# Optimization experiments

Measured on AMD Instinct MI355X. Metric: run time of the kernel, lower is better.

## Reference

```python
import jax, jax.numpy as jnp
import numpy as np

B, S, D, H = 2, 2048, 1024, 16
d = D // H          # per-head dim (chunk along feature dim)
SEQ_LEN = 1024      # config.seq_len mask width
SCALE = float(np.sqrt(D))  # post-softmax divide by sqrt(model_dimension)
LN_EPS = 1e-5


def setup_inputs() -> dict:
    key = jax.random.key(0)
    ks = jax.random.split(key, 10)
    init = lambda k, shape: (jax.random.normal(k, shape, dtype=jnp.float32) * 0.02)
    return {
        "x": jax.random.normal(ks[0], (B, S, D), dtype=jnp.float32),
        "Wq": init(ks[1], (H, d, d)), "bq": jnp.zeros((H, d), jnp.float32),
        "Wk": init(ks[2], (H, d, d)), "bk": jnp.zeros((H, d), jnp.float32),
        "Wv": init(ks[3], (H, d, d)), "bv": jnp.zeros((H, d), jnp.float32),
        "Wo": init(ks[4], (D, D)),    "bo": jnp.zeros((D,), jnp.float32),
        "ln_g": jnp.ones((D,), jnp.float32),
        "ln_b": jnp.zeros((D,), jnp.float32),
    }


def reference(x, Wq, bq, Wk, bk, Wv, bv, Wo, bo, ln_g, ln_b):
    # chunk along feature dim == reshape D -> (H, d) since chunks are contiguous
    xh = x.reshape(B, S, H, d)                                  # [B,S,H,d]
    q = jnp.einsum('bshd,hde->bshe', xh, Wq) + bq               # [B,S,H,d]
    k = jnp.einsum('bshd,hde->bshe', xh, Wk) + bk
    v = jnp.einsum('bshd,hde->bshe', xh, Wv) + bv
    scores = jnp.einsum('bshd,bthd->bhst', q, k)                # [B,H,S,S]
    # custom mask: last query row, last SEQ_LEN key columns -> -inf
    scores = scores.at[:, :, -1, -SEQ_LEN:].set(-jnp.inf)
    attn = jax.nn.softmax(scores, axis=-1) / SCALE              # post-softmax scale
    o = jnp.einsum('bhst,bthd->bshd', attn, v).reshape(B, S, D) # concat heads
    proj = jnp.einsum('bsd,de->bse', o, Wo) + bo                # output projection
    y = x + proj                                                 # residual
    mu = jnp.mean(y, axis=-1, keepdims=True)
    var = jnp.mean(jnp.square(y - mu), axis=-1, keepdims=True)
    return (y - mu) * jax.lax.rsqrt(var + LN_EPS) * ln_g + ln_b
```

## Files before the change

kernel.cpp:

```cpp
#include <hip/hip_runtime.h>
#include <math.h>

#define B 2
#define S 2048
#define D 1024
#define H 16
#define HD 64
#define LN_EPS 1e-5f
#define LOG2E 1.44269504f
#define KSPLIT 2
#define NTS (S / 64 / KSPLIT)
#define NBD_ELEMS (B * S * D)
#define BHS_ELEMS (B * H * S)

typedef __bf16 bf16x8 __attribute__((ext_vector_type(8)));
typedef float f32x4 __attribute__((ext_vector_type(4)));

#if defined(__has_builtin)
#if __has_builtin(__builtin_amdgcn_exp2f)
#define EXP2(x) __builtin_amdgcn_exp2f(x)
#endif
#endif
#ifndef EXP2
#define EXP2(x) __expf((x) * 0.6931471805599453f)
#endif

__device__ __forceinline__ ushort f2bf(float f) {
    uint u = __float_as_uint(f);
    u += 0x7FFFu + ((u >> 16) & 1u);
    return (ushort)(u >> 16);
}

__device__ __forceinline__ bf16x8 ldfrag(const char* base, int row, int cbyte) {
    int a = row * 128 + (cbyte ^ ((row & 7) << 4));
    union { uint4 u; bf16x8 v; } c;
    c.u = *(const uint4*)(base + a);
    return c.v;
}

__device__ __forceinline__ uint comb2(uint a, uint b, float inv) {
    float lo = (__uint_as_float(a << 16) + __uint_as_float(b << 16)) * inv;
    float hi = (__uint_as_float(a & 0xFFFF0000u) + __uint_as_float(b & 0xFFFF0000u)) * inv;
    return (uint)f2bf(lo) | ((uint)f2bf(hi) << 16);
}

__global__ __launch_bounds__(256) void cvt_kernel(
        const float* __restrict__ Wo,
        const float* __restrict__ Wq, const float* __restrict__ Wk,
        const float* __restrict__ Wv,
        ushort* __restrict__ wt, ushort* __restrict__ wqt,
        ushort* __restrict__ wkt, ushort* __restrict__ wvt) {
    __shared__ float t[64][65];
    int tid = threadIdx.x;
    if (blockIdx.y < 16) {
        int r0 = blockIdx.y * 64, c0 = blockIdx.x * 64;
#pragma unroll
        for (int it = 0; it < 16; ++it) {
            int idx = tid + 256 * it;
            int row = idx >> 6, col = idx & 63;
            t[row][col] = Wo[(size_t)(r0 + row) * D + c0 + col];
        }
        __syncthreads();
#pragma unroll
        for (int it = 0; it < 16; ++it) {
            int idx = tid + 256 * it;
            int nrow = idx >> 6, kcol = idx & 63;
            wt[(size_t)(c0 + nrow) * D + r0 + kcol] = f2bf(t[kcol][nrow]);
        }
    } else {
        int h = blockIdx.x, which = blockIdx.y - 16;
        const float* W = (which == 0) ? Wq : (which == 1) ? Wk : Wv;
        ushort* outp = (which == 0) ? wqt : (which == 1) ? wkt : wvt;
        const float* Wh = W + h * HD * HD;
        ushort* oh = outp + h * HD * HD;
#pragma unroll
        for (int it = 0; it < 16; ++it) {
            int idx = tid + 256 * it;
            t[idx >> 6][idx & 63] = Wh[idx];
        }
        __syncthreads();
#pragma unroll
        for (int it = 0; it < 16; ++it) {
            int idx = tid + 256 * it;
            int e = idx >> 6, dd = idx & 63;
            oh[idx] = f2bf(t[dd][e]);
        }
    }
}

__global__ __launch_bounds__(256) void qkv_kernel(
        const float* __restrict__ x,
        const ushort* __restrict__ wqt, const ushort* __restrict__ wkt,
        const ushort* __restrict__ wvt,
        const float* __restrict__ bq, const float* __restrict__ bk,
        const float* __restrict__ bv,
        ushort* __restrict__ qh, ushort* __restrict__ kh, ushort* __restrict__ vth) {
    __shared__ char xt[16384];
    const int tid = threadIdx.x;
    const int w = tid >> 6, l = tid & 63;
    const int lg = l >> 4, lr = l & 15;
    const int h = blockIdx.y;
    const size_t row0 = (size_t)blockIdx.x * 128;
    const int b = (int)(row0 >> 11);
    const int s0 = (int)(row0 & (S - 1));
    const size_t hb = (size_t)b * H + h;

#pragma unroll
    for (int it = 0; it < 4; ++it) {
        int c = tid + 256 * it;
        int row = c >> 3, sub = c & 7;
        const float* src = x + (row0 + row) * D + h * HD + 8 * sub;
        float4 f0 = *(const float4*)src;
        float4 f1 = *(const float4*)(src + 4);
        uint2 lo = make_uint2((uint)f2bf(f0.x) | ((uint)f2bf(f0.y) << 16),
                              (uint)f2bf(f0.z) | ((uint)f2bf(f0.w) << 16));
        uint2 hi = make_uint2((uint)f2bf(f1.x) | ((uint)f2bf(f1.y) << 16),
                              (uint)f2bf(f1.z) | ((uint)f2bf(f1.w) << 16));
        int p0 = 64 * (sub >> 2) + 32 * (sub & 1) + 8 * ((sub >> 1) & 1);
        int sz = (row & 7) << 4;
        char* dst = xt + row * 128;
        *(uint2*)(dst + (p0 ^ sz)) = lo;
        *(uint2*)(dst + ((p0 + 16) ^ sz)) = hi;
    }
    __syncthreads();

    bf16x8 xa[2][2];
#pragma unroll
    for (int fm = 0; fm < 2; ++fm)
#pragma unroll
        for (int ks = 0; ks < 2; ++ks)
            xa[fm][ks] = ldfrag(xt, 32 * w + 16 * fm + lr, 64 * ks + 16 * lg);

#pragma unroll
    for (int tsel = 0; tsel < 3; ++tsel) {
        const ushort* wsrc = (tsel == 0) ? wqt : (tsel == 1) ? wkt : wvt;
        const float* bsrc = (tsel == 0) ? bq : (tsel == 1) ? bk : bv;
        bf16x8 wf[4][2];
#pragma unroll
        for (int fn = 0; fn < 4; ++fn) {
            const char* wp = (const char*)(wsrc + ((size_t)h * HD + 16 * fn + lr) * HD);
#pragma unroll
            for (int ks = 0; ks < 2; ++ks) {
                uint2 a = *(const uint2*)(wp + 64 * ks + 8 * lg);
                uint2 c2 = *(const uint2*)(wp + 64 * ks + 8 * lg + 32);
                union { uint4 u; bf16x8 v; } cc;
                cc.u = make_uint4(a.x, a.y, c2.x, c2.y);
                wf[fn][ks] = cc.v;
            }
        }
        f32x4 acc[2][4];
#pragma unroll
        for (int fm = 0; fm < 2; ++fm)
#pragma unroll
            for (int fn = 0; fn < 4; ++fn)
#pragma unroll
                for (int r = 0; r < 4; ++r) acc[fm][fn][r] = 0.f;
#pragma unroll
        for (int fm = 0; fm < 2; ++fm)
#pragma unroll
            for (int fn = 0; fn < 4; ++fn)
#pragma unroll
                for (int ks = 0; ks < 2; ++ks)
                    acc[fm][fn] = __builtin_amdgcn_mfma_f32_16x16x32_bf16(
                        xa[fm][ks], wf[fn][ks], acc[fm][fn], 0, 0, 0);
        if (tsel == 0) {
#pragma unroll
            for (int fn = 0; fn < 4; ++fn) {
                float bias = bsrc[h * HD + 16 * fn + lr];
#pragma unroll
                for (int fm = 0; fm < 2; ++fm)
#pragma unroll
                    for (int r = 0; r < 4; ++r) {
                        int srow = s0 + 32 * w + 16 * fm + 4 * lg + r;
                        qh[(hb * S + srow) * HD + 16 * fn + lr] =
                            f2bf((acc[fm][fn][r] + bias) * LOG2E);
                    }
            }
        } else if (tsel == 1) {
#pragma unroll
            for (int fn = 0; fn < 4; ++fn) {
                float bias = bsrc[h * HD + 16 * fn + lr];
#pragma unroll
                for (int fm = 0; fm < 2; ++fm)
#pragma unroll
                    for (int r = 0; r < 4; ++r) {
                        int srow = s0 + 32 * w + 16 * fm + 4 * lg + r;
                        kh[(hb * S + srow) * HD + 16 * fn + lr] =
                            f2bf(acc[fm][fn][r] + bias);
                    }
            }
        } else {
#pragma unroll
            for (int fn = 0; fn < 4; ++fn) {
                float bias = bsrc[h * HD + 16 * fn + lr];
                int e = 16 * fn + lr;
#pragma unroll
                for (int fm = 0; fm < 2; ++fm) {
                    uint2 pk;
                    pk.x = (uint)f2bf(acc[fm][fn][0] + bias) |
                           ((uint)f2bf(acc[fm][fn][1] + bias) << 16);
                    pk.y = (uint)f2bf(acc[fm][fn][2] + bias) |
                           ((uint)f2bf(acc[fm][fn][3] + bias) << 16);
                    *(uint2*)(vth + (hb * HD + e) * S + s0 + 32 * w + 16 * fm + 4 * lg) = pk;
                }
            }
        }
    }
}

__global__ __launch_bounds__(256) void attn_kernel(
        const ushort* __restrict__ qh, const ushort* __restrict__ kh,
        const ushort* __restrict__ vth, ushort* __restrict__ ou,
        float* __restrict__ ls) {
    __shared__ char kt[3][8192];
    __shared__ char vt[3][8192];
    const int tid = threadIdx.x;
    const int w = tid >> 6, l = tid & 63;
    const int lg = l >> 4, lr = l & 15;
    const int flat = blockIdx.x + 8 * (blockIdx.y + 2 * blockIdx.z);
    const int xc = flat & 7, sl = flat >> 3;
    const int g = xc + 8 * (sl & 7);
    const int qi = sl >> 3;
    const int ksp = g >> 5;
    const int h = g & (H - 1), b = (g >> 4) & 1;
    const int q0 = qi * 256 + 64 * w;
    const size_t bh = (size_t)b * H + h;
    const ushort* qbase = qh + bh * S * HD;
    const ushort* kbase = kh + bh * S * HD;
    const ushort* vbase = vth + bh * HD * S;

    const int r0s = tid >> 3, ssub = tid & 7;
    const int sp0 = 64 * (ssub >> 2) + 32 * (ssub & 1) + 8 * ((ssub >> 1) & 1);
    const int ssz = (r0s & 7) << 4;

    bf16x8 qf[4][2];
#pragma unroll
    for (int fn = 0; fn < 4; ++fn) {
        const char* qp = (const char*)(qbase + (size_t)(q0 + 16 * fn + lr) * HD);
#pragma unroll
        for (int ks = 0; ks < 2; ++ks) {
            uint2 xlo = *(const uint2*)(qp + 64 * ks + 8 * lg);
            uint2 xhi = *(const uint2*)(qp + 64 * ks + 8 * lg + 32);
            union { uint4 u; bf16x8 v; } c;
            c.u = make_uint4(xlo.x, xlo.y, xhi.x, xhi.y);
            qf[fn][ks] = c.v;
        }
    }

    f32x4 acc[4][4];
#pragma unroll
    for (int fn = 0; fn < 4; ++fn)
#pragma unroll
        for (int n0 = 0; n0 < 4; ++n0)
#pragma unroll
            for (int r = 0; r < 4; ++r) acc[fn][n0][r] = 0.f;
    f32x4 accs[4];
#pragma unroll
    for (int fn = 0; fn < 4; ++fn)
#pragma unroll
        for (int r = 0; r < 4; ++r) accs[fn][r] = 0.f;
    const f32x4 z4 = {0.f, 0.f, 0.f, 0.f};
    bf16x8 onef;
#pragma unroll
    for (int j = 0; j < 8; ++j) onef[j] = (__bf16)1.0f;
    const bool lastq = (q0 + 64 == S) && (lr == 15);

    {
        const int kv0 = ksp * NTS * 64;
#pragma unroll
        for (int it = 0; it < 2; ++it) {
            int row = r0s + 32 * it;
            uint4 kd = *(const uint4*)(kbase + (size_t)(kv0 + row) * HD + 8 * ssub);
            uint4 vd = *(const uint4*)(vbase + (size_t)row * S + kv0 + 8 * ssub);
            char* kr = kt[0] + row * 128;
            char* vr = vt[0] + row * 128;
            *(uint2*)(kr + (sp0 ^ ssz)) = make_uint2(kd.x, kd.y);
            *(uint2*)(kr + ((sp0 + 16) ^ ssz)) = make_uint2(kd.z, kd.w);
            *(uint2*)(vr + (sp0 ^ ssz)) = make_uint2(vd.x, vd.y);
            *(uint2*)(vr + ((sp0 + 16) ^ ssz)) = make_uint2(vd.z, vd.w);
        }
    }
    __syncthreads();

    int cur = 0;
    for (int t = 0; t < NTS; ++t) {
        const int kv0 = (ksp * NTS + t) * 64;
        int nxt = cur + 1; if (nxt == 3) nxt = 0;
        uint4 kd2[2], vd2[2];
        if (t + 1 < NTS) {
#pragma unroll
            for (int it = 0; it < 2; ++it) {
                int row = r0s + 32 * it;
                kd2[it] = *(const uint4*)(kbase + (size_t)(kv0 + 64 + row) * HD + 8 * ssub);
                vd2[it] = *(const uint4*)(vbase + (size_t)row * S + kv0 + 64 + 8 * ssub);
            }
        }

        const char* ktb = kt[cur];
        const char* vtb = vt[cur];
        __builtin_amdgcn_s_setprio(1);
        bf16x8 pa[4][2];
#pragma unroll
        for (int half = 0; half < 2; ++half) {
            f32x4 s2[2][4];
#pragma unroll
            for (int fm2 = 0; fm2 < 2; ++fm2) {
                int fm = 2 * half + fm2;
                bf16x8 k0 = ldfrag(ktb, fm * 16 + lr, 16 * lg);
                bf16x8 k1 = ldfrag(ktb, fm * 16 + lr, 64 + 16 * lg);
#pragma unroll
                for (int fn = 0; fn < 4; ++fn) {
                    s2[fm2][fn] = __builtin_amdgcn_mfma_f32_16x16x32_bf16(k0, qf[fn][0], z4, 0, 0, 0);
                    s2[fm2][fn] = __builtin_amdgcn_mfma_f32_16x16x32_bf16(k1, qf[fn][1], s2[fm2][fn], 0, 0, 0);
                }
            }
            if (lastq && kv0 >= S - 1024) {
#pragma unroll
                for (int fm2 = 0; fm2 < 2; ++fm2)
#pragma unroll
                    for (int r = 0; r < 4; ++r) s2[fm2][3][r] = -INFINITY;
            }
#pragma unroll
            for (int fn = 0; fn < 4; ++fn)
#pragma unroll
                for (int j = 0; j < 8; ++j)
                    pa[fn][half][j] = (__bf16)EXP2(s2[j >> 2][fn][j & 3]);
        }
#pragma unroll
        for (int fn = 0; fn < 4; ++fn) {
            accs[fn] = __builtin_amdgcn_mfma_f32_16x16x32_bf16(pa[fn][0], onef, accs[fn], 0, 0, 0);
            accs[fn] = __builtin_amdgcn_mfma_f32_16x16x32_bf16(pa[fn][1], onef, accs[fn], 0, 0, 0);
        }
#pragma unroll
        for (int n0 = 0; n0 < 4; ++n0) {
            bf16x8 v0 = ldfrag(vtb, n0 * 16 + lr, 16 * lg);
            bf16x8 v1 = ldfrag(vtb, n0 * 16 + lr, 64 + 16 * lg);
#pragma unroll
            for (int fn = 0; fn < 4; ++fn) {
                acc[fn][n0] = __builtin_amdgcn_mfma_f32_16x16x32_bf16(pa[fn][0], v0, acc[fn][n0], 0, 0, 0);
                acc[fn][n0] = __builtin_amdgcn_mfma_f32_16x16x32_bf16(pa[fn][1], v1, acc[fn][n0], 0, 0, 0);
            }
        }
        __builtin_amdgcn_s_setprio(0);

        if (t + 1 < NTS) {
#pragma unroll
            for (int it = 0; it < 2; ++it) {
                int row = r0s + 32 * it;
                char* kr = kt[nxt] + row * 128;
                char* vr = vt[nxt] + row * 128;
                *(uint2*)(kr + (sp0 ^ ssz)) = make_uint2(kd2[it].x, kd2[it].y);
                *(uint2*)(kr + ((sp0 + 16) ^ ssz)) = make_uint2(kd2[it].z, kd2[it].w);
                *(uint2*)(vr + (sp0 ^ ssz)) = make_uint2(vd2[it].x, vd2[it].y);
                *(uint2*)(vr + ((sp0 + 16) ^ ssz)) = make_uint2(vd2[it].z, vd2[it].w);
            }
            __syncthreads();
        }
        cur = nxt;
    }

#pragma unroll
    for (int fn = 0; fn < 4; ++fn)
#pragma unroll
        for (int r = 0; r < 4; ++r) {
            int qrow = q0 + 16 * fn + 4 * lg + r;
            ushort* op = ou + (((size_t)ksp * B + b) * S + qrow) * D + h * HD;
#pragma unroll
            for (int n0 = 0; n0 < 4; ++n0)
                op[n0 * 16 + lr] = f2bf(acc[fn][n0][r]);
            if (lr == 0)
                ls[(((size_t)ksp * B + b) * H + h) * S + qrow] = accs[fn][r];
        }
}

__global__ __launch_bounds__(256) void proj_gemm_kernel(
        const ushort* __restrict__ ou, const float* __restrict__ ls,
        const ushort* __restrict__ wt,
        const float* __restrict__ x, const float* __restrict__ bo,
        float* __restrict__ yws) {
    __shared__ char at[3][8192];
    __shared__ char btl[3][16384];
    const int tid = threadIdx.x;
    const int w = tid >> 6, l = tid & 63;
    const int lg = l >> 4, lr = l & 15;
    const int wr = w >> 1, wc = w & 1;
    const int flat = blockIdx.x + 8 * blockIdx.y;
    const int xc = flat & 7, sl = flat >> 3;
    const int m0 = (xc + 8 * (sl & 7)) * 64;
    const int n0 = (sl >> 3) * 128;

    const ushort* srcA[2];
    const float* lsp[2];
    int offA1[2], offA2[2];
#pragma unroll
    for (int it = 0; it < 2; ++it) {
        int c = tid + 256 * it;
        int row = c >> 3, sub = c & 7;
        int r = m0 + row;
        srcA[it] = ou + (size_t)r * D + 8 * sub;
        int b = r >> 11, s = r & (S - 1);
        lsp[it] = ls + (size_t)b * H * S + s;
        int p0 = 64 * (sub >> 2) + 32 * (sub & 1) + 8 * ((sub >> 1) & 1);
        int sz = (row & 7) << 4;
        offA1[it] = row * 128 + (p0 ^ sz);
        offA2[it] = row * 128 + ((p0 + 16) ^ sz);
    }
    const ushort* srcB[4];
    int offB1[4], offB2[4];
#pragma unroll
    for (int it = 0; it < 4; ++it) {
        int c = tid + 256 * it;
        int row = c >> 3, sub = c & 7;
        srcB[it] = wt + (size_t)(n0 + row) * D + 8 * sub;
        int p0 = 64 * (sub >> 2) + 32 * (sub & 1) + 8 * ((sub >> 1) & 1);
        int sz = (row & 7) << 4;
        offB1[it] = row * 128 + (p0 ^ sz);
        offB2[it] = row * 128 + ((p0 + 16) ^ sz);
    }

    f32x4 acc[2][4];
#pragma unroll
    for (int fm = 0; fm < 2; ++fm)
#pragma unroll
        for (int fn = 0; fn < 4; ++fn)
#pragma unroll
            for (int r = 0; r < 4; ++r) acc[fm][fn][r] = 0.f;

    uint4 pa0[2], pa1[2], pb[4];
    float pl0[2], pl1[2];

    auto LOADT = [&](int t) {
#pragma unroll
        for (int it = 0; it < 2; ++it) {
            pa0[it] = *(const uint4*)(srcA[it] + (size_t)t * 64);
            pa1[it] = *(const uint4*)(srcA[it] + (size_t)NBD_ELEMS + (size_t)t * 64);
            pl0[it] = lsp[it][(size_t)t * S];
            pl1[it] = lsp[it][(size_t)BHS_ELEMS + (size_t)t * S];
        }
#pragma unroll
        for (int it = 0; it < 4; ++it)
            pb[it] = *(const uint4*)(srcB[it] + (size_t)t * 64);
    };
    auto STORET = [&](int buf) {
#pragma unroll
        for (int it = 0; it < 2; ++it) {
            float inv = 1.0f / ((pl0[it] + pl1[it]) * 32.0f);
            uint cx = comb2(pa0[it].x, pa1[it].x, inv);
            uint cy = comb2(pa0[it].y, pa1[it].y, inv);
            uint cz = comb2(pa0[it].z, pa1[it].z, inv);
            uint cw = comb2(pa0[it].w, pa1[it].w, inv);
            *(uint2*)(at[buf] + offA1[it]) = make_uint2(cx, cy);
            *(uint2*)(at[buf] + offA2[it]) = make_uint2(cz, cw);
        }
#pragma unroll
        for (int it = 0; it < 4; ++it) {
            *(uint2*)(btl[buf] + offB1[it]) = make_uint2(pb[it].x, pb[it].y);
            *(uint2*)(btl[buf] + offB2[it]) = make_uint2(pb[it].z, pb[it].w);
        }
    };

    LOADT(0);
    STORET(0);
    __syncthreads();

    int cur = 0;
    for (int t = 0; t < D / 64; ++t) {
        int nxt = cur + 1; if (nxt == 3) nxt = 0;
        if (t + 1 < D / 64) LOADT(t + 1);

        bf16x8 af[2][2], bfr[4][2];
#pragma unroll
        for (int fm = 0; fm < 2; ++fm)
#pragma unroll
            for (int ks = 0; ks < 2; ++ks)
                af[fm][ks] = ldfrag(at[cur], 32 * wr + 16 * fm + lr, 64 * ks + 16 * lg);
#pragma unroll
        for (int fn = 0; fn < 4; ++fn)
#pragma unroll
            for (int ks = 0; ks < 2; ++ks)
                bfr[fn][ks] = ldfrag(btl[cur], 64 * wc + 16 * fn + lr, 64 * ks + 16 * lg);
#pragma unroll
        for (int fm = 0; fm < 2; ++fm)
#pragma unroll
            for (int fn = 0; fn < 4; ++fn)
#pragma unroll
                for (int ks = 0; ks < 2; ++ks)
                    acc[fm][fn] = __builtin_amdgcn_mfma_f32_16x16x32_bf16(
                        af[fm][ks], bfr[fn][ks], acc[fm][fn], 0, 0, 0);

        if (t + 1 < D / 64) {
            STORET(nxt);
            __syncthreads();
        }
        cur = nxt;
    }

#pragma unroll
    for (int fm = 0; fm < 2; ++fm)
#pragma unroll
        for (int fn = 0; fn < 4; ++fn) {
            int col = n0 + 64 * wc + 16 * fn + lr;
            float bov = bo[col];
#pragma unroll
            for (int r = 0; r < 4; ++r) {
                int rowg = m0 + 32 * wr + 16 * fm + 4 * lg + r;
                size_t off = (size_t)rowg * D + col;
                yws[off] = acc[fm][fn][r] + x[off] + bov;
            }
        }
}

__global__ __launch_bounds__(256) void ln_kernel(
        const float* __restrict__ yws, const float* __restrict__ g,
        const float* __restrict__ bb, float* __restrict__ out) {
    __shared__ float rs[4], rq[4];
    int tid = threadIdx.x;
    size_t row = blockIdx.x;
    float4 yv = *(const float4*)(yws + row * D + tid * 4);
    float s = yv.x + yv.y + yv.z + yv.w;
    float q = yv.x * yv.x + yv.y * yv.y + yv.z * yv.z + yv.w * yv.w;
    for (int off = 32; off > 0; off >>= 1) {
        s += __shfl_down(s, off, 64);
        q += __shfl_down(q, off, 64);
    }
    if ((tid & 63) == 0) { rs[tid >> 6] = s; rq[tid >> 6] = q; }
    __syncthreads();
    float sum = rs[0] + rs[1] + rs[2] + rs[3];
    float sq  = rq[0] + rq[1] + rq[2] + rq[3];
    float mean = sum * (1.0f / D);
    float var  = sq * (1.0f / D) - mean * mean;
    float rstd = rsqrtf(var + LN_EPS);
    float4 gv = *(const float4*)(g + tid * 4);
    float4 bv = *(const float4*)(bb + tid * 4);
    float4 ov;
    ov.x = (yv.x - mean) * rstd * gv.x + bv.x;
    ov.y = (yv.y - mean) * rstd * gv.y + bv.y;
    ov.z = (yv.z - mean) * rstd * gv.z + bv.z;
    ov.w = (yv.w - mean) * rstd * gv.w + bv.w;
    *(float4*)(out + row * D + tid * 4) = ov;
}

extern "C" void kernel_launch(void* const* d_in, const int* in_sizes, int n_in,
                              void* d_out, int out_size, void* d_ws, size_t ws_size,
                              hipStream_t stream) {
    const float* x  = (const float*)d_in[0];
    const float* Wq = (const float*)d_in[1];
    const float* bq = (const float*)d_in[2];
    const float* Wk = (const float*)d_in[3];
    const float* bk = (const float*)d_in[4];
    const float* Wv = (const float*)d_in[5];
    const float* bv = (const float*)d_in[6];
    const float* Wo = (const float*)d_in[7];
    const float* bo = (const float*)d_in[8];
    const float* g  = (const float*)d_in[9];
    const float* bb = (const float*)d_in[10];
    float* out = (float*)d_out;

    const size_t NBD = (size_t)B * S * D;
    ushort* qh  = (ushort*)d_ws;
    ushort* kh  = qh + NBD;
    ushort* vth = kh + NBD;
    ushort* wt  = vth + NBD;
    ushort* wqt = wt + (size_t)D * D;
    ushort* wkt = wqt + H * HD * HD;
    ushort* wvt = wkt + H * HD * HD;
    ushort* ou  = wvt + H * HD * HD;
    float*  ls  = (float*)(ou + (size_t)KSPLIT * NBD);
    float*  yws = (float*)d_ws;

    cvt_kernel<<<dim3(16, 19), 256, 0, stream>>>(Wo, Wq, Wk, Wv, wt, wqt, wkt, wvt);
    qkv_kernel<<<dim3((B * S) / 128, H), 256, 0, stream>>>(
        x, wqt, wkt, wvt, bq, bk, bv, qh, kh, vth);
    attn_kernel<<<dim3(S / 256, KSPLIT, H * B), 256, 0, stream>>>(qh, kh, vth, ou, ls);
    proj_gemm_kernel<<<dim3(D / 128, (B * S) / 64), 256, 0, stream>>>(ou, ls, wt, x, bo, yws);
    ln_kernel<<<dim3(B * S), 256, 0, stream>>>(yws, g, bb, out);
}
```

Measured before the change: 98.34 us.

## Enlarge attention blocks to 512 threads and split keys four ways

Each attention workgroup grows to 8 waves covering 512 queries, so every staged K/V tile is shared by twice as many waves. The key dimension is now split into four partitions instead of two, which keeps the total number of workgroups the same. The projection GEMM is changed to sum four partial outputs and four row-sum partials before normalising. In exchange, the partial output buffer and the reads in the projection prologue double, and larger workgroups may lower occupancy.

```diff
diff --git a/kernel.cpp b/kernel.cpp
--- a/kernel.cpp
+++ b/kernel.cpp
@@ -8,7 +8,8 @@
 #define HD 64
 #define LN_EPS 1e-5f
 #define LOG2E 1.44269504f
-#define KSPLIT 2
+#define KSPLIT 4
+#define QB 512
 #define NTS (S / 64 / KSPLIT)
 #define NBD_ELEMS (B * S * D)
 #define BHS_ELEMS (B * H * S)
@@ -38,9 +39,11 @@
     return c.v;
 }
 
-__device__ __forceinline__ uint comb2(uint a, uint b, float inv) {
-    float lo = (__uint_as_float(a << 16) + __uint_as_float(b << 16)) * inv;
-    float hi = (__uint_as_float(a & 0xFFFF0000u) + __uint_as_float(b & 0xFFFF0000u)) * inv;
+__device__ __forceinline__ uint comb4(uint a, uint b, uint c, uint d, float inv) {
+    float lo = (__uint_as_float(a << 16) + __uint_as_float(b << 16) +
+                __uint_as_float(c << 16) + __uint_as_float(d << 16)) * inv;
+    float hi = (__uint_as_float(a & 0xFFFF0000u) + __uint_as_float(b & 0xFFFF0000u) +
+                __uint_as_float(c & 0xFFFF0000u) + __uint_as_float(d & 0xFFFF0000u)) * inv;
     return (uint)f2bf(lo) | ((uint)f2bf(hi) << 16);
 }
 
@@ -208,7 +211,7 @@
     }
 }
 
-__global__ __launch_bounds__(256) void attn_kernel(
+__global__ __launch_bounds__(512) void attn_kernel(
         const ushort* __restrict__ qh, const ushort* __restrict__ kh,
         const ushort* __restrict__ vth, ushort* __restrict__ ou,
         float* __restrict__ ls) {
@@ -217,13 +220,13 @@
     const int tid = threadIdx.x;
     const int w = tid >> 6, l = tid & 63;
     const int lg = l >> 4, lr = l & 15;
-    const int flat = blockIdx.x + 8 * (blockIdx.y + 2 * blockIdx.z);
+    const int flat = blockIdx.x + 4 * (blockIdx.y + KSPLIT * blockIdx.z);
     const int xc = flat & 7, sl = flat >> 3;
-    const int g = xc + 8 * (sl & 7);
-    const int qi = sl >> 3;
+    const int g = xc + 8 * (sl & 15);
+    const int qi = sl >> 4;
     const int ksp = g >> 5;
     const int h = g & (H - 1), b = (g >> 4) & 1;
-    const int q0 = qi * 256 + 64 * w;
+    const int q0 = qi * QB + 64 * w;
     const size_t bh = (size_t)b * H + h;
     const ushort* qbase = qh + bh * S * HD;
     const ushort* kbase = kh + bh * S * HD;
@@ -267,18 +270,14 @@
 
     {
         const int kv0 = ksp * NTS * 64;
-#pragma unroll
-        for (int it = 0; it < 2; ++it) {
-            int row = r0s + 32 * it;
-            uint4 kd = *(const uint4*)(kbase + (size_t)(kv0 + row) * HD + 8 * ssub);
-            uint4 vd = *(const uint4*)(vbase + (size_t)row * S + kv0 + 8 * ssub);
-            char* kr = kt[0] + row * 128;
-            char* vr = vt[0] + row * 128;
-            *(uint2*)(kr + (sp0 ^ ssz)) = make_uint2(kd.x, kd.y);
-            *(uint2*)(kr + ((sp0 + 16) ^ ssz)) = make_uint2(kd.z, kd.w);
-            *(uint2*)(vr + (sp0 ^ ssz)) = make_uint2(vd.x, vd.y);
-            *(uint2*)(vr + ((sp0 + 16) ^ ssz)) = make_uint2(vd.z, vd.w);
-        }
+        uint4 kd = *(const uint4*)(kbase + (size_t)(kv0 + r0s) * HD + 8 * ssub);
+        uint4 vd = *(const uint4*)(vbase + (size_t)r0s * S + kv0 + 8 * ssub);
+        char* kr = kt[0] + r0s * 128;
+        char* vr = vt[0] + r0s * 128;
+        *(uint2*)(kr + (sp0 ^ ssz)) = make_uint2(kd.x, kd.y);
+        *(uint2*)(kr + ((sp0 + 16) ^ ssz)) = make_uint2(kd.z, kd.w);
+        *(uint2*)(vr + (sp0 ^ ssz)) = make_uint2(vd.x, vd.y);
+        *(uint2*)(vr + ((sp0 + 16) ^ ssz)) = make_uint2(vd.z, vd.w);
     }
     __syncthreads();
 
@@ -286,14 +285,10 @@
     for (int t = 0; t < NTS; ++t) {
         const int kv0 = (ksp * NTS + t) * 64;
         int nxt = cur + 1; if (nxt == 3) nxt = 0;
-        uint4 kd2[2], vd2[2];
+        uint4 kd2, vd2;
         if (t + 1 < NTS) {
-#pragma unroll
-            for (int it = 0; it < 2; ++it) {
-                int row = r0s + 32 * it;
-                kd2[it] = *(const uint4*)(kbase + (size_t)(kv0 + 64 + row) * HD + 8 * ssub);
-                vd2[it] = *(const uint4*)(vbase + (size_t)row * S + kv0 + 64 + 8 * ssub);
-            }
+            kd2 = *(const uint4*)(kbase + (size_t)(kv0 + 64 + r0s) * HD + 8 * ssub);
+            vd2 = *(const uint4*)(vbase + (size_t)r0s * S + kv0 + 64 + 8 * ssub);
         }
 
         const char* ktb = kt[cur];
@@ -344,16 +339,12 @@
         __builtin_amdgcn_s_setprio(0);
 
         if (t + 1 < NTS) {
-#pragma unroll
-            for (int it = 0; it < 2; ++it) {
-                int row = r0s + 32 * it;
-                char* kr = kt[nxt] + row * 128;
-                char* vr = vt[nxt] + row * 128;
-                *(uint2*)(kr + (sp0 ^ ssz)) = make_uint2(kd2[it].x, kd2[it].y);
-                *(uint2*)(kr + ((sp0 + 16) ^ ssz)) = make_uint2(kd2[it].z, kd2[it].w);
-                *(uint2*)(vr + (sp0 ^ ssz)) = make_uint2(vd2[it].x, vd2[it].y);
-                *(uint2*)(vr + ((sp0 + 16) ^ ssz)) = make_uint2(vd2[it].z, vd2[it].w);
-            }
+            char* kr = kt[nxt] + r0s * 128;
+            char* vr = vt[nxt] + r0s * 128;
+            *(uint2*)(kr + (sp0 ^ ssz)) = make_uint2(kd2.x, kd2.y);
+            *(uint2*)(kr + ((sp0 + 16) ^ ssz)) = make_uint2(kd2.z, kd2.w);
+            *(uint2*)(vr + (sp0 ^ ssz)) = make_uint2(vd2.x, vd2.y);
+            *(uint2*)(vr + ((sp0 + 16) ^ ssz)) = make_uint2(vd2.z, vd2.w);
             __syncthreads();
         }
         cur = nxt;
@@ -426,16 +417,17 @@
 #pragma unroll
             for (int r = 0; r < 4; ++r) acc[fm][fn][r] = 0.f;
 
-    uint4 pa0[2], pa1[2], pb[4];
-    float pl0[2], pl1[2];
+    uint4 pa[KSPLIT][2], pb[4];
+    float pl[KSPLIT][2];
 
     auto LOADT = [&](int t) {
 #pragma unroll
         for (int it = 0; it < 2; ++it) {
-            pa0[it] = *(const uint4*)(srcA[it] + (size_t)t * 64);
-            pa1[it] = *(const uint4*)(srcA[it] + (size_t)NBD_ELEMS + (size_t)t * 64);
-            pl0[it] = lsp[it][(size_t)t * S];
-            pl1[it] = lsp[it][(size_t)BHS_ELEMS + (size_t)t * S];
+#pragma unroll
+            for (int k = 0; k < KSPLIT; ++k) {
+                pa[k][it] = *(const uint4*)(srcA[it] + (size_t)k * NBD_ELEMS + (size_t)t * 64);
+                pl[k][it] = lsp[it][(size_t)k * BHS_ELEMS + (size_t)t * S];
+            }
         }
 #pragma unroll
         for (int it = 0; it < 4; ++it)
@@ -444,11 +436,12 @@
     auto STORET = [&](int buf) {
 #pragma unroll
         for (int it = 0; it < 2; ++it) {
-            float inv = 1.0f / ((pl0[it] + pl1[it]) * 32.0f);
-            uint cx = comb2(pa0[it].x, pa1[it].x, inv);
-            uint cy = comb2(pa0[it].y, pa1[it].y, inv);
-            uint cz = comb2(pa0[it].z, pa1[it].z, inv);
-            uint cw = comb2(pa0[it].w, pa1[it].w, inv);
+            float inv = 1.0f /
+                ((pl[0][it] + pl[1][it] + pl[2][it] + pl[3][it]) * 32.0f);
+            uint cx = comb4(pa[0][it].x, pa[1][it].x, pa[2][it].x, pa[3][it].x, inv);
+            uint cy = comb4(pa[0][it].y, pa[1][it].y, pa[2][it].y, pa[3][it].y, inv);
+            uint cz = comb4(pa[0][it].z, pa[1][it].z, pa[2][it].z, pa[3][it].z, inv);
+            uint cw = comb4(pa[0][it].w, pa[1][it].w, pa[2][it].w, pa[3][it].w, inv);
             *(uint2*)(at[buf] + offA1[it]) = make_uint2(cx, cy);
             *(uint2*)(at[buf] + offA2[it]) = make_uint2(cz, cw);
         }
@@ -571,7 +564,7 @@
     cvt_kernel<<<dim3(16, 19), 256, 0, stream>>>(Wo, Wq, Wk, Wv, wt, wqt, wkt, wvt);
     qkv_kernel<<<dim3((B * S) / 128, H), 256, 0, stream>>>(
         x, wqt, wkt, wvt, bq, bk, bv, qh, kh, vth);
-    attn_kernel<<<dim3(S / 256, KSPLIT, H * B), 256, 0, stream>>>(qh, kh, vth, ou, ls);
+    attn_kernel<<<dim3(S / QB, KSPLIT, H * B), 512, 0, stream>>>(qh, kh, vth, ou, ls);
     proj_gemm_kernel<<<dim3(D / 128, (B * S) / 64), 256, 0, stream>>>(ou, ls, wt, x, bo, yws);
     ln_kernel<<<dim3(B * S), 256, 0, stream>>>(yws, g, bb, out);
 }
```

Result: slower. 109.0 us (+10.9%).
